# Performance work log

Measured on AMD Instinct MI355X. Metric: run time of the kernel, lower is better.

Reference implementation:

```python
import jax, jax.numpy as jnp
import numpy as np

B, S, V, E, H, L = 2, 2048, 32000, 512, 512, 3


def _layernorm(x, w, b, eps=1e-5):
    m = jnp.mean(x, axis=-1, keepdims=True)
    v = jnp.var(x, axis=-1, keepdims=True)
    y = (x - m) * jax.lax.rsqrt(v + eps) * w
    return y if b is None else y + b


def _log_g(x):
    # log of g(x) = where(x>=0, x+0.5, sigmoid(x)) used by minGRU/minLSTM
    return jnp.where(x >= 0, jnp.log(jax.nn.relu(x) + 0.5), -jax.nn.softplus(-x))


def _parallel_scan_log(log_coeffs, log_values):
    # log_coeffs: (B,S,H) log forget gates; log_values: (B,S+1,H) [log h0, log(i*h_tilde)]
    a_star = jnp.cumsum(jnp.pad(log_coeffs, ((0, 0), (1, 0), (0, 0))), axis=1)  # (B,S+1,H)
    log_h = a_star + jax.lax.cumlogsumexp(log_values - a_star, axis=1)
    return jnp.exp(log_h)[:, 1:]  # (B,S,H)


def _forward(ids, emb, Ws, bs, ln_w, ln_b, fln_w, fc_w, fc_b):
    x = emb[ids]  # (B,S,E) embedding gather
    log_h0 = jnp.full((x.shape[0], 1, H), jnp.log(0.5), dtype=x.dtype)  # h0 = g(0) = 0.5
    for l in range(L):
        inp = x
        xn = _layernorm(x, ln_w[l], ln_b[l])  # pre-norm
        gates = jnp.einsum('bsd,gd->bsg', xn, Ws[l]) + bs[l]  # (B,S,3H)
        f_g, i_g, tilde = jnp.split(gates, 3, axis=-1)
        # minLSTM normalized gates in log space: f' = sigma(f)/(sigma(f)+sigma(i))
        diff = jax.nn.softplus(-f_g) - jax.nn.softplus(-i_g)
        log_f = -jax.nn.softplus(diff)
        log_i = -jax.nn.softplus(-diff)
        log_vals = jnp.concatenate([log_h0, log_i + _log_g(tilde)], axis=1)
        h = _parallel_scan_log(log_f, log_vals)  # (B,S,H)
        x = h + inp  # residual (dims match)
    x = _layernorm(x, fln_w, None)  # final LayerNorm, bias=False
    logits = jnp.einsum('bsh,vh->bsv', x, fc_w) + fc_b
    return logits


def setup_inputs() -> dict:
    key = jax.random.key(0)
    ks = jax.random.split(key, 9)
    return {
        'ids': jax.random.randint(ks[0], (B, S), 0, V, dtype=jnp.int32),
        'emb': jax.random.normal(ks[1], (V, E), dtype=jnp.float32) * 0.02,
        'Ws': jax.random.normal(ks[2], (L, 3 * H, H), dtype=jnp.float32) * 0.02,
        'bs': jax.random.normal(ks[3], (L, 3 * H), dtype=jnp.float32) * 0.02,
        'ln_w': 1.0 + 0.01 * jax.random.normal(ks[4], (L, H), dtype=jnp.float32),
        'ln_b': 0.01 * jax.random.normal(ks[5], (L, H), dtype=jnp.float32),
        'fln_w': 1.0 + 0.01 * jax.random.normal(ks[6], (H,), dtype=jnp.float32),
        'fc_w': jax.random.normal(ks[7], (V, H), dtype=jnp.float32) * 0.02,
        'fc_b': jax.random.normal(ks[8], (V,), dtype=jnp.float32) * 0.02,
    }


def reference(ids, emb, Ws, bs, ln_w, ln_b, fln_w, fc_w, fc_b):
    return _forward(ids, emb, Ws, bs, ln_w, ln_b, fln_w, fc_w, fc_b)
```

## Files before the change

### kernel.cpp

```cpp
#include <hip/hip_runtime.h>
#include <stdint.h>

#define BB 2
#define SS 2048
#define VV 32000
#define HH 512
#define LL 3
#define ROWS (BB * SS)
#define G3 (3 * HH)

#define NCHUNK 64
#define CLEN (SS / NCHUNK)

typedef __attribute__((ext_vector_type(8))) __bf16 bf16x8;
typedef __attribute__((ext_vector_type(4))) float f32x4;

__device__ __forceinline__ unsigned short f2bf(float f) {
    union { float f; unsigned int u; } cv; cv.f = f;
    unsigned int u = cv.u;
    u += 0x7fffu + ((u >> 16) & 1u);
    return (unsigned short)(u >> 16);
}

__device__ __forceinline__ void gl2lds16(const void* g, void* l) {
    __builtin_amdgcn_global_load_lds(
        (__attribute__((address_space(1))) void*)g,
        (__attribute__((address_space(3))) void*)l, 16, 0, 0);
}

__global__ __launch_bounds__(256) void embed_k(const int* __restrict__ ids,
                                               const float* __restrict__ emb,
                                               float* __restrict__ x) {
    int idx = blockIdx.x * blockDim.x + threadIdx.x;
    int row = idx >> 7;
    int c4  = idx & 127;
    int id = ids[row];
    *(float4*)(x + (size_t)row * HH + c4 * 4) =
        *(const float4*)(emb + (size_t)id * HH + c4 * 4);
}

__global__ __launch_bounds__(256) void tobf16_k(const float* __restrict__ in,
                                                unsigned short* __restrict__ outp,
                                                int n4) {
    int i = blockIdx.x * blockDim.x + threadIdx.x;
    if (i >= n4) return;
    float4 v = *(const float4*)(in + (size_t)i * 4);
    unsigned short o[4] = { f2bf(v.x), f2bf(v.y), f2bf(v.z), f2bf(v.w) };
    *(uint2*)(outp + (size_t)i * 4) = *(uint2*)o;
}

__global__ __launch_bounds__(256) void ln_k(const float* __restrict__ x,
                                            const float* __restrict__ w,
                                            const float* __restrict__ b,
                                            unsigned short* __restrict__ xn) {
    int wid  = (blockIdx.x * blockDim.x + threadIdx.x) >> 6;
    int lane = threadIdx.x & 63;
    if (wid >= ROWS) return;
    const float* xr = x + (size_t)wid * HH;
    float4 v0 = *(const float4*)(xr + lane * 8);
    float4 v1 = *(const float4*)(xr + lane * 8 + 4);
    float vs[8] = { v0.x, v0.y, v0.z, v0.w, v1.x, v1.y, v1.z, v1.w };
    float s = 0.f, q = 0.f;
#pragma unroll
    for (int j = 0; j < 8; j++) { s += vs[j]; q += vs[j] * vs[j]; }
#pragma unroll
    for (int off = 32; off; off >>= 1) {
        s += __shfl_xor(s, off);
        q += __shfl_xor(q, off);
    }
    float mean = s * (1.f / HH);
    float var  = q * (1.f / HH) - mean * mean;
    float r    = rsqrtf(var + 1e-5f);
    unsigned short o[8];
#pragma unroll
    for (int j = 0; j < 8; j++) {
        float wj = w[lane * 8 + j];
        float bj = b ? b[lane * 8 + j] : 0.f;
        o[j] = f2bf((vs[j] - mean) * r * wj + bj);
    }
    *(uint4*)(xn + (size_t)wid * HH + lane * 8) = *(uint4*)o;
}

#define BM 128
#define BN 128
#define BK 32
#define MT (ROWS / BM)
#define SCPAD 68

__global__ __launch_bounds__(256) void gemm_bt(const unsigned short* __restrict__ A,
                                               const unsigned short* __restrict__ Bt,
                                               const float* __restrict__ bias,
                                               float* __restrict__ C,
                                               int K, int ldc) {
    __shared__ __align__(16) char smem[4 * 16 * SCPAD * 4];
    unsigned short* lA = (unsigned short*)smem;
    unsigned short* lB = lA + BM * BK;

    int nwg = gridDim.x;
    int wg = blockIdx.x;
    if ((nwg & 7) == 0) { int q = nwg >> 3; wg = (wg & 7) * q + (wg >> 3); }
    int m0 = (wg % MT) * BM;
    int n0 = (wg / MT) * BN;

    int t = threadIdx.x;
    int lane = t & 63;
    int w = t >> 6;
    int wm = (w >> 1) * 64, wn = (w & 1) * 64;

    f32x4 acc[4][4];
#pragma unroll
    for (int i = 0; i < 4; i++)
#pragma unroll
        for (int j = 0; j < 4; j++) acc[i][j] = (f32x4){0.f, 0.f, 0.f, 0.f};

    int r0 = t >> 2, c0 = (t & 3) * 8;
    const unsigned short* pa0 = A  + (size_t)(m0 + r0) * K + c0;
    const unsigned short* pa1 = A  + (size_t)(m0 + r0 + 64) * K + c0;
    const unsigned short* pb0 = Bt + (size_t)(n0 + r0) * K + c0;
    const unsigned short* pb1 = Bt + (size_t)(n0 + r0 + 64) * K + c0;
    unsigned short* dA0 = lA + (w * 64) * 8;
    unsigned short* dA1 = lA + (256 + w * 64) * 8;
    unsigned short* dB0 = lB + (w * 64) * 8;
    unsigned short* dB1 = lB + (256 + w * 64) * 8;

    int fm = lane & 15;
    int fq = (lane >> 4) * 8;
    const unsigned short* paf = lA + (wm + fm) * BK + fq;
    const unsigned short* pbf = lB + (wn + fm) * BK + fq;

    int nkt = K / BK;
    for (int kt = 0; kt < nkt; kt++) {
        gl2lds16(pa0, dA0);
        gl2lds16(pa1, dA1);
        gl2lds16(pb0, dB0);
        gl2lds16(pb1, dB1);
        pa0 += BK; pa1 += BK; pb0 += BK; pb1 += BK;
        __syncthreads();
        bf16x8 af[4], bfr[4];
#pragma unroll
        for (int i = 0; i < 4; i++) af[i] = *(const bf16x8*)(paf + i * 16 * BK);
#pragma unroll
        for (int j = 0; j < 4; j++) bfr[j] = *(const bf16x8*)(pbf + j * 16 * BK);
#pragma unroll
        for (int i = 0; i < 4; i++)
#pragma unroll
            for (int j = 0; j < 4; j++)
                acc[i][j] = __builtin_amdgcn_mfma_f32_16x16x32_bf16(
                    af[i], bfr[j], acc[i][j], 0, 0, 0);
        __syncthreads();
    }

    float* sc = (float*)(smem + w * 16 * SCPAD * 4);
    int cl = lane & 15, qh = lane >> 4;
    int gcol = n0 + wn + cl * 4;
    float4 bb = bias ? *(const float4*)(bias + gcol)
                     : make_float4(0.f, 0.f, 0.f, 0.f);
#pragma unroll
    for (int i = 0; i < 4; i++) {
#pragma unroll
        for (int j = 0; j < 4; j++)
#pragma unroll
            for (int r = 0; r < 4; r++)
                sc[(qh * 4 + r) * SCPAD + j * 16 + cl] = acc[i][j][r];
#pragma unroll
        for (int rr = 0; rr < 4; rr++) {
            int lrow = rr * 4 + qh;
            float4 v = *(float4*)(sc + lrow * SCPAD + cl * 4);
            v.x += bb.x; v.y += bb.y; v.z += bb.z; v.w += bb.w;
            *(float4*)(C + (size_t)(m0 + wm + i * 16 + lrow) * ldc + gcol) = v;
        }
    }
}

__global__ __launch_bounds__(256) void scan1_k(float* __restrict__ gates,
                                               float* __restrict__ Ach,
                                               float* __restrict__ Bch) {
    int tid = blockIdx.x * blockDim.x + threadIdx.x;
    int ch = tid & (BB * HH - 1);
    int c  = tid >> 10;
    int b = ch >> 9, h = ch & (HH - 1);
    float a = 1.f, acc = 0.f;
    size_t base = ((size_t)b * SS + (size_t)c * CLEN) * G3 + h;
    for (int s = 0; s < CLEN; s++) {
        float fg = gates[base];
        float ig = gates[base + HH];
        float tg = gates[base + 2 * HH];
        float sf = 1.f / (1.f + expf(-fg));
        float si = 1.f / (1.f + expf(-ig));
        float inv = 1.f / (sf + si);
        float fp = sf * inv;
        float ip = si * inv;
        float g  = tg >= 0.f ? tg + 0.5f : 1.f / (1.f + expf(-tg));
        float v  = ip * g;
        gates[base] = fp;
        gates[base + HH] = v;
        a = fp * a;
        acc = fp * acc + v;
        base += G3;
    }
    Ach[tid] = a;
    Bch[tid] = acc;
}

__global__ __launch_bounds__(256) void scan2_k(const float* __restrict__ Ach,
                                               const float* __restrict__ Bch,
                                               float* __restrict__ hin) {
    int ch = blockIdx.x * blockDim.x + threadIdx.x;
    float hh = 0.5f;
    for (int c = 0; c < NCHUNK; c++) {
        int i = c * (BB * HH) + ch;
        hin[i] = hh;
        hh = Ach[i] * hh + Bch[i];
    }
}

__global__ __launch_bounds__(256) void scan3_k(const float* __restrict__ gates,
                                               const float* __restrict__ hin,
                                               float* __restrict__ x) {
    int tid = blockIdx.x * blockDim.x + threadIdx.x;
    int ch = tid & (BB * HH - 1);
    int c  = tid >> 10;
    int b = ch >> 9, h = ch & (HH - 1);
    float hh = hin[c * (BB * HH) + ch];
    size_t gbase = ((size_t)b * SS + (size_t)c * CLEN) * G3 + h;
    size_t xbase = ((size_t)b * SS + (size_t)c * CLEN) * HH + h;
    for (int s = 0; s < CLEN; s++) {
        float fp = gates[gbase];
        float v  = gates[gbase + HH];
        hh = fp * hh + v;
        x[xbase] += hh;
        gbase += G3;
        xbase += HH;
    }
}

extern "C" void kernel_launch(void* const* d_in, const int* in_sizes, int n_in,
                              void* d_out, int out_size, void* d_ws, size_t ws_size,
                              hipStream_t stream) {
    const int*   ids  = (const int*)  d_in[0];
    const float* emb  = (const float*)d_in[1];
    const float* Ws   = (const float*)d_in[2];
    const float* bs   = (const float*)d_in[3];
    const float* lnw  = (const float*)d_in[4];
    const float* lnb  = (const float*)d_in[5];
    const float* flnw = (const float*)d_in[6];
    const float* fcw  = (const float*)d_in[7];
    const float* fcb  = (const float*)d_in[8];
    float* out = (float*)d_out;

    char* p = (char*)d_ws;
    float* x            = (float*)p;           p += (size_t)ROWS * HH * 4;
    unsigned short* xnb = (unsigned short*)p;  p += (size_t)ROWS * HH * 2;
    unsigned short* wsb = (unsigned short*)p;  p += (size_t)LL * G3 * HH * 2;
    unsigned short* fwb = (unsigned short*)p;  p += (size_t)VV * HH * 2;
    float* gates        = (float*)p;           p += (size_t)ROWS * G3 * 4;
    float* Ach          = (float*)p;           p += (size_t)NCHUNK * BB * HH * 4;
    float* Bch          = (float*)p;           p += (size_t)NCHUNK * BB * HH * 4;
    float* hin          = (float*)p;           p += (size_t)NCHUNK * BB * HH * 4;

    embed_k<<<ROWS * (HH / 4) / 256, 256, 0, stream>>>(ids, emb, x);
    tobf16_k<<<(LL * G3 * HH / 4 + 255) / 256, 256, 0, stream>>>(Ws, wsb, LL * G3 * HH / 4);
    tobf16_k<<<(VV * HH / 4 + 255) / 256, 256, 0, stream>>>(fcw, fwb, VV * HH / 4);

    for (int l = 0; l < LL; l++) {
        ln_k<<<ROWS / 4, 256, 0, stream>>>(x, lnw + l * HH, lnb + l * HH, xnb);
        gemm_bt<<<MT * (G3 / BN), 256, 0, stream>>>(
            xnb, wsb + (size_t)l * G3 * HH, bs + l * G3, gates, HH, G3);
        scan1_k<<<NCHUNK * BB * HH / 256, 256, 0, stream>>>(gates, Ach, Bch);
        scan2_k<<<BB * HH / 256, 256, 0, stream>>>(Ach, Bch, hin);
        scan3_k<<<NCHUNK * BB * HH / 256, 256, 0, stream>>>(gates, hin, x);
    }

    ln_k<<<ROWS / 4, 256, 0, stream>>>(x, flnw, nullptr, xnb);
    gemm_bt<<<MT * (VV / BN), 256, 0, stream>>>(xnb, fwb, fcb, out, HH, VV);
}
```

Baseline: 970.0 us.

## Add 256x256-tile pipelined bf16 MFMA GEMM for final vocab projection

Adds a new GEMM kernel with 256x256 output tiles, 512 threads, and double-buffered async global-to-LDS staging. It interleaves MFMA phases with barriers, priority hints and swizzled LDS layout, and remaps workgroups for cache locality. It replaces the generic GEMM for the large logits projection to increase data reuse and overlap loads with compute. The kernel hardcodes K=512 and M=4096 tile counts and needs 128KB of shared memory per block.

```diff
diff --git a/kernel.cpp b/kernel.cpp
--- a/kernel.cpp
+++ b/kernel.cpp
@@ -168,6 +168,132 @@
             float4 v = *(float4*)(sc + lrow * SCPAD + cl * 4);
             v.x += bb.x; v.y += bb.y; v.z += bb.z; v.w += bb.w;
             *(float4*)(C + (size_t)(m0 + wm + i * 16 + lrow) * ldc + gcol) = v;
+        }
+    }
+}
+
+#define REGION(buf, mat, kk) ((((buf) * 2 + (mat)) * 2 + (kk)) * 16384)
+#define WAITVM(n) asm volatile("s_waitcnt vmcnt(" #n ")" ::: "memory")
+
+#define STAGE(tt, mat, kk) do { \
+    char* d_ = smem + REGION((tt) & 1, mat, kk) + w * 2048; \
+    const unsigned short* s0_ = (mat ? gB0 : gA0) + (tt) * 64 + (kk) * 32; \
+    const unsigned short* s1_ = (mat ? gB1 : gA1) + (tt) * 64 + (kk) * 32; \
+    gl2lds16(s0_, d_); \
+    gl2lds16(s1_, d_ + 1024); \
+} while (0)
+
+#define MFMA4(OH, i4, av) do { \
+    acc[(OH)*4+(i4)][0] = __builtin_amdgcn_mfma_f32_16x16x32_bf16(av, bq0, acc[(OH)*4+(i4)][0], 0, 0, 0); \
+    acc[(OH)*4+(i4)][1] = __builtin_amdgcn_mfma_f32_16x16x32_bf16(av, bq1, acc[(OH)*4+(i4)][1], 0, 0, 0); \
+    acc[(OH)*4+(i4)][2] = __builtin_amdgcn_mfma_f32_16x16x32_bf16(av, bq2, acc[(OH)*4+(i4)][2], 0, 0, 0); \
+    acc[(OH)*4+(i4)][3] = __builtin_amdgcn_mfma_f32_16x16x32_bf16(av, bq3, acc[(OH)*4+(i4)][3], 0, 0, 0); \
+} while (0)
+
+#define PHASE(T, KK, OH, READB, STAGE_STMT, WAIT_STMT) do { \
+    const char* Ab_ = smem + REGION((T) & 1, 0, KK) + aoff; \
+    const char* Bb_ = smem + REGION((T) & 1, 1, KK) + boff; \
+    bf16x8 a0_ = *(const bf16x8*)(Ab_ + ((OH)*4 + 0) * 1024); \
+    bf16x8 a1_ = *(const bf16x8*)(Ab_ + ((OH)*4 + 1) * 1024); \
+    bf16x8 a2_ = *(const bf16x8*)(Ab_ + ((OH)*4 + 2) * 1024); \
+    bf16x8 a3_ = *(const bf16x8*)(Ab_ + ((OH)*4 + 3) * 1024); \
+    if (READB) { \
+        bq0 = *(const bf16x8*)(Bb_ + 0 * 1024); \
+        bq1 = *(const bf16x8*)(Bb_ + 1 * 1024); \
+        bq2 = *(const bf16x8*)(Bb_ + 2 * 1024); \
+        bq3 = *(const bf16x8*)(Bb_ + 3 * 1024); \
+    } \
+    STAGE_STMT; \
+    WAIT_STMT; \
+    __builtin_amdgcn_sched_barrier(0); \
+    __builtin_amdgcn_s_barrier(); \
+    asm volatile("s_waitcnt lgkmcnt(0)" ::: "memory"); \
+    __builtin_amdgcn_sched_barrier(0); \
+    __builtin_amdgcn_s_setprio(1); \
+    MFMA4(OH, 0, a0_); MFMA4(OH, 1, a1_); MFMA4(OH, 2, a2_); MFMA4(OH, 3, a3_); \
+    __builtin_amdgcn_s_setprio(0); \
+    __builtin_amdgcn_sched_barrier(0); \
+    __builtin_amdgcn_s_barrier(); \
+} while (0)
+
+__global__ __launch_bounds__(512, 2) void gemm256(const unsigned short* __restrict__ A,
+                                                  const unsigned short* __restrict__ Bt,
+                                                  const float* __restrict__ bias,
+                                                  float* __restrict__ C, int ldc) {
+    __shared__ __align__(16) char smem[131072];
+
+    int nwg = gridDim.x;
+    int wg = blockIdx.x;
+    if ((nwg & 7) == 0) { int q = nwg >> 3; wg = (wg & 7) * q + (wg >> 3); }
+    int m0 = (wg & 15) * 256;
+    int n0 = (wg >> 4) * 256;
+
+    int tid = threadIdx.x;
+    int lane = tid & 63;
+    int w = tid >> 6;
+    int wave_m = w >> 2, wave_n = w & 3;
+
+    int fm = lane & 15;
+    int fq16 = (lane >> 4) * 16;
+    int lsw = (fm * 64 + fq16) ^ ((fm & 8) ? 32 : 0);
+    int aoff = wave_m * 8192 + lsw;
+    int boff = wave_n * 4096 + lsw;
+
+    int ep = (lane * 8) ^ ((lane & 32) ? 16 : 0);
+    int row_l = ep >> 5, kc_l = ep & 31;
+    const unsigned short* gA0 = A  + (size_t)(m0 + w * 32 + row_l) * 512 + kc_l;
+    const unsigned short* gA1 = gA0 + 16 * 512;
+    const unsigned short* gB0 = Bt + (size_t)(n0 + w * 32 + row_l) * 512 + kc_l;
+    const unsigned short* gB1 = gB0 + 16 * 512;
+
+    f32x4 acc[8][4];
+#pragma unroll
+    for (int i = 0; i < 8; i++)
+#pragma unroll
+        for (int j = 0; j < 4; j++) acc[i][j] = (f32x4){0.f, 0.f, 0.f, 0.f};
+    bf16x8 bq0, bq1, bq2, bq3;
+
+    STAGE(0, 0, 0); STAGE(0, 1, 0); STAGE(0, 0, 1); STAGE(0, 1, 1);
+    STAGE(1, 0, 0); STAGE(1, 1, 0);
+    WAITVM(8);
+    __builtin_amdgcn_sched_barrier(0);
+    __builtin_amdgcn_s_barrier();
+
+#pragma unroll
+    for (int t = 0; t < 8; ++t) {
+        PHASE(t, 0, 0, 1,
+              if (t < 7) STAGE(t + 1, 0, 1),
+              (void)0);
+        PHASE(t, 0, 1, 0,
+              if (t < 7) STAGE(t + 1, 1, 1),
+              if (t < 7) { WAITVM(8); } else { WAITVM(0); });
+        PHASE(t, 1, 0, 1,
+              if (t < 6) STAGE(t + 2, 0, 0),
+              (void)0);
+        PHASE(t, 1, 1, 0,
+              if (t < 6) STAGE(t + 2, 1, 0),
+              if (t < 6) { WAITVM(8); } else if (t == 6) { WAITVM(4); });
+    }
+
+    asm volatile("" ::: "memory");
+    float* sc = (float*)(smem + w * 16 * SCPAD * 4);
+    int cl = fm, qh = lane >> 4;
+    int gcol = n0 + wave_n * 64 + cl * 4;
+    float4 bb = bias ? *(const float4*)(bias + gcol)
+                     : make_float4(0.f, 0.f, 0.f, 0.f);
+#pragma unroll
+    for (int i = 0; i < 8; ++i) {
+#pragma unroll
+        for (int j = 0; j < 4; ++j)
+#pragma unroll
+            for (int r = 0; r < 4; ++r)
+                sc[(qh * 4 + r) * SCPAD + j * 16 + cl] = acc[i][j][r];
+#pragma unroll
+        for (int rr = 0; rr < 4; ++rr) {
+            int lrow = rr * 4 + qh;
+            float4 v = *(float4*)(sc + lrow * SCPAD + cl * 4);
+            v.x += bb.x; v.y += bb.y; v.z += bb.z; v.w += bb.w;
+            *(float4*)(C + (size_t)(m0 + wave_m * 128 + i * 16 + lrow) * ldc + gcol) = v;
         }
     }
 }
@@ -272,5 +398,5 @@
     }
 
     ln_k<<<ROWS / 4, 256, 0, stream>>>(x, flnw, nullptr, xnb);
-    gemm_bt<<<MT * (VV / BN), 256, 0, stream>>>(xnb, fwb, fcb, out, HH, VV);
-}
+    gemm256<<<16 * (VV / 256), 512, 0, stream>>>(xnb, fwb, fcb, out, VV);
+}
```

After: 931.6 us. 1.04x faster.
